# Kernel tuning notes

Measured on AMD Instinct MI355X. Metric: run time of the kernel, lower is better.

The kernel has to match this reference:

```python
import jax, jax.numpy as jnp
import numpy as np

E = 100  # embed_size


def _forward_sentence(noun_emb, subj_cube, obj_cube, words, vs, vo, vt):
    # words: [W] noun ids; vs/vo: [N,2]; vt: [N,3]
    word_sum = noun_emb[words].sum(axis=0)  # [E]
    # gather verb matrices (rows of E*E) in the original cat order
    verb_mats = jnp.concatenate([
        subj_cube[vs[:, 0]],
        obj_cube[vo[:, 0]],
        subj_cube[vt[:, 0]],
        obj_cube[vt[:, 0]],
    ], axis=0).reshape(-1, E, E)  # [4N, E, E]
    arg_vecs = jnp.concatenate([
        noun_emb[vs[:, 1]],
        noun_emb[vo[:, 1]],
        noun_emb[vt[:, 1]],
        noun_emb[vt[:, 2]],
    ], axis=0)  # [4N, E]
    # batched matrix-vector product then reduce over all edges
    verb_arg_sum = jnp.einsum('nij,nj->i', verb_mats, arg_vecs)  # [E]
    return word_sum + verb_arg_sum


def setup_inputs() -> dict:
    key = jax.random.key(0)
    ks = jax.random.split(key, 16)
    n_nouns, n_verbs, hidden = 100000, 5000, 300
    inp = {
        'words1': jax.random.randint(ks[0], (50000,), 0, n_nouns),
        'verb_subj1': jax.random.randint(ks[1], (5000, 2), 0, n_verbs),
        'verb_obj1': jax.random.randint(ks[2], (5000, 2), 0, n_verbs),
        'verb_trans1': jax.random.randint(ks[3], (5000, 3), 0, n_verbs),
        'words2': jax.random.randint(ks[4], (50000,), 0, n_nouns),
        'verb_subj2': jax.random.randint(ks[5], (5000, 2), 0, n_verbs),
        'verb_obj2': jax.random.randint(ks[6], (5000, 2), 0, n_verbs),
        'verb_trans2': jax.random.randint(ks[7], (5000, 3), 0, n_verbs),
        'noun_emb': jax.random.normal(ks[8], (n_nouns, E), jnp.float32) * 0.1,
        'subj_cube': jax.random.normal(ks[9], (n_verbs, E * E), jnp.float32) * 0.02,
        'obj_cube': jax.random.normal(ks[10], (n_verbs, E * E), jnp.float32) * 0.02,
        'W_h': jax.random.normal(ks[11], (hidden, 4 * E), jnp.float32) * 0.05,
        'b_h': jax.random.normal(ks[12], (hidden,), jnp.float32) * 0.05,
        'W_o': jax.random.normal(ks[13], (3, hidden), jnp.float32) * 0.05,
        'b_o': jax.random.normal(ks[14], (3,), jnp.float32) * 0.05,
    }
    return inp


def reference(words1, verb_subj1, verb_obj1, verb_trans1,
              words2, verb_subj2, verb_obj2, verb_trans2,
              noun_emb, subj_cube, obj_cube, W_h, b_h, W_o, b_o):
    emb1 = _forward_sentence(noun_emb, subj_cube, obj_cube, words1, verb_subj1, verb_obj1, verb_trans1)
    emb2 = _forward_sentence(noun_emb, subj_cube, obj_cube, words2, verb_subj2, verb_obj2, verb_trans2)
    mult_dist = emb1 * emb2
    abs_dist = jnp.abs(emb1 - emb2)
    vec_dist = jnp.concatenate([emb1, emb2, mult_dist, abs_dist], axis=0)  # [4E]
    h = jax.nn.sigmoid(vec_dist @ W_h.T + b_h)  # [hidden]
    out = jax.nn.log_softmax(h @ W_o.T + b_o, axis=-1)  # [3]
    return out
```

## Files before the change

### kernel.cpp

```cpp
#include <hip/hip_runtime.h>
#include <math.h>

#define E 100
#define NV 5000
#define NPART 64
#define CAP 16


__global__ void init_kernel(int* __restrict__ count, float* __restrict__ partial) {
    int p = blockIdx.x * blockDim.x + threadIdx.x;
    if (p < 4 * NV) count[p] = 0;
    if (p < NPART * 2 * E) partial[p] = 0.f;
}

__global__ void bucket_build_kernel(const int* __restrict__ vs1, const int* __restrict__ vo1,
                                    const int* __restrict__ vt1,
                                    const int* __restrict__ vs2, const int* __restrict__ vo2,
                                    const int* __restrict__ vt2,
                                    int* __restrict__ count, int* __restrict__ bucket) {
    int p = blockIdx.x * blockDim.x + threadIdx.x;
    if (p >= 40000) return;
    int sent = p / 20000;
    int r = p - sent * 20000;
    int kind = r / 5000;
    int idx = r - kind * 5000;
    const int* vs = sent ? vs2 : vs1;
    const int* vo = sent ? vo2 : vo1;
    const int* vt = sent ? vt2 : vt1;
    int verb, arg, cube;
    if (kind == 0)      { verb = vs[idx * 2]; arg = vs[idx * 2 + 1]; cube = 0; }
    else if (kind == 1) { verb = vo[idx * 2]; arg = vo[idx * 2 + 1]; cube = 1; }
    else if (kind == 2) { verb = vt[idx * 3]; arg = vt[idx * 3 + 1]; cube = 0; }
    else                { verb = vt[idx * 3]; arg = vt[idx * 3 + 2]; cube = 1; }
    int slot = (cube * 2 + sent) * NV + verb;
    int pos = atomicAdd(&count[slot], 1);
    if (pos < CAP) bucket[slot * CAP + pos] = arg;
}

__global__ __launch_bounds__(512) void word_sum_kernel(const int* __restrict__ w1,
                                                       const int* __restrict__ w2,
                                                       const float* __restrict__ noun_emb,
                                                       float* __restrict__ partial) {
    __shared__ int wid[400];
    __shared__ float wred[E];
    int b = blockIdx.x;
    int sent = b / 125;
    int cb = b - sent * 125;
    const int* words = sent ? w2 : w1;
    int t = threadIdx.x;
    if (t < 400) wid[t] = words[cb * 400 + t];
    if (t >= 400 && t < 500) wred[t - 400] = 0.f;
    __syncthreads();
    if (t < 500) {
        int wl = t / 25, k = t - (t / 25) * 25;
        const float4* ne4 = (const float4*)noun_emb;
        float ax = 0.f, ay = 0.f, az = 0.f, aw = 0.f;
        #pragma unroll
        for (int j = 0; j < 20; j++) {
            float4 v = ne4[wid[wl * 20 + j] * 25 + k];
            ax += v.x; ay += v.y; az += v.z; aw += v.w;
        }
        atomicAdd(&wred[k * 4 + 0], ax);
        atomicAdd(&wred[k * 4 + 1], ay);
        atomicAdd(&wred[k * 4 + 2], az);
        atomicAdd(&wred[k * 4 + 3], aw);
    }
    __syncthreads();
    if (t < 100) atomicAdd(&partial[((b & (NPART - 1)) * 2 + sent) * E + t], wred[t]);
}

__global__ __launch_bounds__(512) void cube_pass_kernel(const float* __restrict__ subj,
                                                        const float* __restrict__ obj,
                                                        const float* __restrict__ noun_emb,
                                                        const int* __restrict__ count,
                                                        const int* __restrict__ bucket,
                                                        float* __restrict__ partial) {
    __shared__ float xs[5][2][E];
    __shared__ float yred[2][E];

    int b = blockIdx.x;
    int cube = b / 1000;
    int vbase = (b - cube * 1000) * 5;
    int t = threadIdx.x;

    if (t < 200) yred[t / 100][t % 100] = 0.f;

    if (t < 500) {
        int g = t / 100, i = t - (t / 100) * 100;
        #pragma unroll
        for (int s = 0; s < 2; s++) {
            int slot = (cube * 2 + s) * NV + vbase + g;
            int n = count[slot]; if (n > CAP) n = CAP;
            const int4* b4 = (const int4*)(bucket + slot * CAP);
            int4 q0 = b4[0], q1 = b4[1], q2 = b4[2], q3 = b4[3];
            int ids[16] = {q0.x,q0.y,q0.z,q0.w, q1.x,q1.y,q1.z,q1.w,
                           q2.x,q2.y,q2.z,q2.w, q3.x,q3.y,q3.z,q3.w};
            float acc = 0.f;
            #pragma unroll
            for (int j = 0; j < CAP; j++)
                if (j < n) acc += noun_emb[ids[j] * E + i];
            xs[g][s][i] = acc;
        }
    }
    __syncthreads();

    if (t < 500) {
        int tr = t / 25, c = t - (t / 25) * 25;
        float4 xf1[5], xf2[5];
        #pragma unroll
        for (int v = 0; v < 5; v++) {
            xf1[v] = *(const float4*)&xs[v][0][c * 4];
            xf2[v] = *(const float4*)&xs[v][1][c * 4];
        }
        const float* cb = cube ? obj : subj;
        const float4* base = (const float4*)cb + (size_t)vbase * 2500;
        #pragma unroll
        for (int it = 0; it < 5; it++) {
            float a1 = 0.f, a2 = 0.f;
            #pragma unroll
            for (int v = 0; v < 5; v++) {
                float4 m = base[v * 2500 + it * 500 + t];
                a1 += m.x * xf1[v].x + m.y * xf1[v].y + m.z * xf1[v].z + m.w * xf1[v].w;
                a2 += m.x * xf2[v].x + m.y * xf2[v].y + m.z * xf2[v].z + m.w * xf2[v].w;
            }
            int row = it * 20 + tr;
            atomicAdd(&yred[0][row], a1);
            atomicAdd(&yred[1][row], a2);
        }
    }
    __syncthreads();

    if (t < 200) {
        int s = t / 100, i = t - (t / 100) * 100;
        atomicAdd(&partial[((b & (NPART - 1)) * 2 + s) * E + i], yred[s][i]);
    }
}

__global__ __launch_bounds__(512) void hidden_kernel(const float* __restrict__ partial,
                                                     const float* __restrict__ W_h,
                                                     const float* __restrict__ b_h,
                                                     float* __restrict__ hbuf) {
    __shared__ float vds[4 * E];
    int t = threadIdx.x;
    if (t < 200) {
        int s = t / 100, i = t - (t / 100) * 100;
        float sum = 0.f;
        #pragma unroll 8
        for (int p = 0; p < NPART; p++) sum += partial[(p * 2 + s) * E + i];
        vds[s * E + i] = sum;
    }
    __syncthreads();
    if (t < E) {
        float e1 = vds[t], e2 = vds[E + t];
        vds[2 * E + t] = e1 * e2;
        vds[3 * E + t] = fabsf(e1 - e2);
    }
    __syncthreads();
    int wave = t >> 6, lane = t & 63;
    int h = blockIdx.x * 8 + wave;
    if (h < 300) {
        const float4* w4 = (const float4*)(W_h + (size_t)h * 4 * E);
        const float4* v4 = (const float4*)vds;
        float4 w = w4[lane], v = v4[lane];
        float acc = w.x * v.x + w.y * v.y + w.z * v.z + w.w * v.w;
        if (lane < 36) {
            float4 w2 = w4[lane + 64], v2 = v4[lane + 64];
            acc += w2.x * v2.x + w2.y * v2.y + w2.z * v2.z + w2.w * v2.w;
        }
        #pragma unroll
        for (int off = 32; off > 0; off >>= 1) acc += __shfl_down(acc, off);
        if (lane == 0) hbuf[h] = 1.f / (1.f + expf(-(acc + b_h[h])));
    }
}

__global__ __launch_bounds__(512) void out_kernel(const float* __restrict__ hbuf,
                                                  const float* __restrict__ W_o,
                                                  const float* __restrict__ b_o,
                                                  float* __restrict__ out) {
    __shared__ float hs[300];
    __shared__ float o[3];
    int t = threadIdx.x;
    if (t < 300) hs[t] = hbuf[t];
    __syncthreads();
    int wave = t >> 6, lane = t & 63;
    if (wave < 3) {
        float acc = 0.f;
        #pragma unroll
        for (int j = 0; j < 5; j++) {
            int h = lane + j * 64;
            if (h < 300) acc += W_o[wave * 300 + h] * hs[h];
        }
        #pragma unroll
        for (int off = 32; off > 0; off >>= 1) acc += __shfl_down(acc, off);
        if (lane == 0) o[wave] = acc + b_o[wave];
    }
    __syncthreads();
    if (t == 0) {
        float m = fmaxf(o[0], fmaxf(o[1], o[2]));
        float l = logf(expf(o[0] - m) + expf(o[1] - m) + expf(o[2] - m)) + m;
        out[0] = o[0] - l;
        out[1] = o[1] - l;
        out[2] = o[2] - l;
    }
}

extern "C" void kernel_launch(void* const* d_in, const int* in_sizes, int n_in,
                              void* d_out, int out_size, void* d_ws, size_t ws_size,
                              hipStream_t stream) {
    const int* words1 = (const int*)d_in[0];
    const int* vs1    = (const int*)d_in[1];
    const int* vo1    = (const int*)d_in[2];
    const int* vt1    = (const int*)d_in[3];
    const int* words2 = (const int*)d_in[4];
    const int* vs2    = (const int*)d_in[5];
    const int* vo2    = (const int*)d_in[6];
    const int* vt2    = (const int*)d_in[7];
    const float* noun_emb = (const float*)d_in[8];
    const float* subj     = (const float*)d_in[9];
    const float* obj      = (const float*)d_in[10];
    const float* W_h      = (const float*)d_in[11];
    const float* b_h      = (const float*)d_in[12];
    const float* W_o      = (const float*)d_in[13];
    const float* b_o      = (const float*)d_in[14];
    float* out = (float*)d_out;

    int*   count   = (int*)d_ws;
    int*   bucket  = count + 4 * NV;
    float* partial = (float*)(bucket + 4 * NV * CAP);
    float* hbuf    = partial + NPART * 2 * E;

    init_kernel<<<(4 * NV + 255) / 256, 256, 0, stream>>>(count, partial);
    bucket_build_kernel<<<(40000 + 255) / 256, 256, 0, stream>>>(
        vs1, vo1, vt1, vs2, vo2, vt2, count, bucket);
    word_sum_kernel<<<250, 512, 0, stream>>>(words1, words2, noun_emb, partial);
    cube_pass_kernel<<<2000, 512, 0, stream>>>(subj, obj, noun_emb, count, bucket, partial);
    hidden_kernel<<<38, 512, 0, stream>>>(partial, W_h, b_h, hbuf);
    out_kernel<<<1, 512, 0, stream>>>(hbuf, W_o, b_o, out);
}
```

Before: 469.9 us.

## Precompute argument-sum vectors and stream cube rows one thread per row

Adds a separate kernel that gathers and sums the noun embeddings for each verb slot into a dense buffer A. The fused cube kernel is replaced by a streaming kernel in which each thread computes one 100-wide row dot product against both sentences' A vectors. The goal is to drop the shared-memory staging and block syncs and let more blocks stream the 400 MB of verb cubes. In exchange, each lane reads its own contiguous 400-byte row, so loads within a wavefront are not coalesced across lanes. Every thread also issues its own global atomicAdds into the partial buffer instead of reducing within the block first.

Result: slower. 542.3 us (+15.4%).

```diff
diff --git a/kernel.cpp b/kernel.cpp
--- a/kernel.cpp
+++ b/kernel.cpp
@@ -37,6 +37,27 @@
     if (pos < CAP) bucket[slot * CAP + pos] = arg;
 }
 
+__global__ void build_A_kernel(const int* __restrict__ count, const int* __restrict__ bucket,
+                               const float* __restrict__ noun_emb, float* __restrict__ A) {
+    int p = blockIdx.x * blockDim.x + threadIdx.x;
+    if (p >= 4 * NV * 25) return;
+    int slot = p / 25, c = p - (p / 25) * 25;
+    int n = count[slot]; if (n > CAP) n = CAP;
+    const int4* b4 = (const int4*)(bucket + slot * CAP);
+    int4 q0 = b4[0], q1 = b4[1], q2 = b4[2], q3 = b4[3];
+    int ids[16] = {q0.x,q0.y,q0.z,q0.w, q1.x,q1.y,q1.z,q1.w,
+                   q2.x,q2.y,q2.z,q2.w, q3.x,q3.y,q3.z,q3.w};
+    const float4* ne4 = (const float4*)noun_emb;
+    float ax = 0.f, ay = 0.f, az = 0.f, aw = 0.f;
+    #pragma unroll
+    for (int j = 0; j < CAP; j++)
+        if (j < n) {
+            float4 v = ne4[ids[j] * 25 + c];
+            ax += v.x; ay += v.y; az += v.z; aw += v.w;
+        }
+    ((float4*)A)[p] = make_float4(ax, ay, az, aw);
+}
+
 __global__ __launch_bounds__(512) void word_sum_kernel(const int* __restrict__ w1,
                                                        const int* __restrict__ w2,
                                                        const float* __restrict__ noun_emb,
@@ -69,71 +90,39 @@
     if (t < 100) atomicAdd(&partial[((b & (NPART - 1)) * 2 + sent) * E + t], wred[t]);
 }
 
-__global__ __launch_bounds__(512) void cube_pass_kernel(const float* __restrict__ subj,
-                                                        const float* __restrict__ obj,
-                                                        const float* __restrict__ noun_emb,
-                                                        const int* __restrict__ count,
-                                                        const int* __restrict__ bucket,
-                                                        float* __restrict__ partial) {
-    __shared__ float xs[5][2][E];
-    __shared__ float yred[2][E];
-
-    int b = blockIdx.x;
-    int cube = b / 1000;
-    int vbase = (b - cube * 1000) * 5;
-    int t = threadIdx.x;
-
-    if (t < 200) yred[t / 100][t % 100] = 0.f;
-
-    if (t < 500) {
-        int g = t / 100, i = t - (t / 100) * 100;
-        #pragma unroll
-        for (int s = 0; s < 2; s++) {
-            int slot = (cube * 2 + s) * NV + vbase + g;
-            int n = count[slot]; if (n > CAP) n = CAP;
-            const int4* b4 = (const int4*)(bucket + slot * CAP);
-            int4 q0 = b4[0], q1 = b4[1], q2 = b4[2], q3 = b4[3];
-            int ids[16] = {q0.x,q0.y,q0.z,q0.w, q1.x,q1.y,q1.z,q1.w,
-                           q2.x,q2.y,q2.z,q2.w, q3.x,q3.y,q3.z,q3.w};
-            float acc = 0.f;
-            #pragma unroll
-            for (int j = 0; j < CAP; j++)
-                if (j < n) acc += noun_emb[ids[j] * E + i];
-            xs[g][s][i] = acc;
-        }
-    }
-    __syncthreads();
-
-    if (t < 500) {
-        int tr = t / 25, c = t - (t / 25) * 25;
-        float4 xf1[5], xf2[5];
-        #pragma unroll
-        for (int v = 0; v < 5; v++) {
-            xf1[v] = *(const float4*)&xs[v][0][c * 4];
-            xf2[v] = *(const float4*)&xs[v][1][c * 4];
-        }
-        const float* cb = cube ? obj : subj;
-        const float4* base = (const float4*)cb + (size_t)vbase * 2500;
-        #pragma unroll
-        for (int it = 0; it < 5; it++) {
-            float a1 = 0.f, a2 = 0.f;
-            #pragma unroll
-            for (int v = 0; v < 5; v++) {
-                float4 m = base[v * 2500 + it * 500 + t];
-                a1 += m.x * xf1[v].x + m.y * xf1[v].y + m.z * xf1[v].z + m.w * xf1[v].w;
-                a2 += m.x * xf2[v].x + m.y * xf2[v].y + m.z * xf2[v].z + m.w * xf2[v].w;
-            }
-            int row = it * 20 + tr;
-            atomicAdd(&yred[0][row], a1);
-            atomicAdd(&yred[1][row], a2);
-        }
-    }
-    __syncthreads();
-
-    if (t < 200) {
-        int s = t / 100, i = t - (t / 100) * 100;
-        atomicAdd(&partial[((b & (NPART - 1)) * 2 + s) * E + i], yred[s][i]);
-    }
+__global__ __launch_bounds__(256, 4) void cube_stream_kernel(const float* __restrict__ subj,
+                                                             const float* __restrict__ obj,
+                                                             const float* __restrict__ A,
+                                                             float* __restrict__ partial) {
+    int r = blockIdx.x * 256 + threadIdx.x;
+    if (r >= 2 * NV * E) return;
+    int cube = r / (NV * E);
+    int rem = r - cube * (NV * E);
+    int v = rem / E, i = rem - v * E;
+    const float4* row = (const float4*)(cube ? obj : subj) + (size_t)rem * 25;
+    const float4* x1  = (const float4*)A + ((size_t)(cube * 2 + 0) * NV + v) * 25;
+    const float4* x2  = (const float4*)A + ((size_t)(cube * 2 + 1) * NV + v) * 25;
+
+    float a1e = 0.f, a1o = 0.f, a2e = 0.f, a2o = 0.f;
+    #pragma unroll
+    for (int k = 0; k < 24; k += 2) {
+        float4 m0 = row[k],   m1 = row[k + 1];
+        float4 p0 = x1[k],    p1 = x1[k + 1];
+        float4 q0 = x2[k],    q1 = x2[k + 1];
+        a1e += m0.x * p0.x + m0.y * p0.y + m0.z * p0.z + m0.w * p0.w;
+        a1o += m1.x * p1.x + m1.y * p1.y + m1.z * p1.z + m1.w * p1.w;
+        a2e += m0.x * q0.x + m0.y * q0.y + m0.z * q0.z + m0.w * q0.w;
+        a2o += m1.x * q1.x + m1.y * q1.y + m1.z * q1.z + m1.w * q1.w;
+    }
+    {
+        float4 m0 = row[24];
+        float4 p0 = x1[24], q0 = x2[24];
+        a1e += m0.x * p0.x + m0.y * p0.y + m0.z * p0.z + m0.w * p0.w;
+        a2e += m0.x * q0.x + m0.y * q0.y + m0.z * q0.z + m0.w * q0.w;
+    }
+    int sl = (blockIdx.x & (NPART - 1)) * 2;
+    atomicAdd(&partial[(sl + 0) * E + i], a1e + a1o);
+    atomicAdd(&partial[(sl + 1) * E + i], a2e + a2o);
 }
 
 __global__ __launch_bounds__(512) void hidden_kernel(const float* __restrict__ partial,
@@ -226,14 +215,16 @@
 
     int*   count   = (int*)d_ws;
     int*   bucket  = count + 4 * NV;
-    float* partial = (float*)(bucket + 4 * NV * CAP);
+    float* A       = (float*)(bucket + 4 * NV * CAP);
+    float* partial = A + 4 * NV * E;
     float* hbuf    = partial + NPART * 2 * E;
 
     init_kernel<<<(4 * NV + 255) / 256, 256, 0, stream>>>(count, partial);
     bucket_build_kernel<<<(40000 + 255) / 256, 256, 0, stream>>>(
         vs1, vo1, vt1, vs2, vo2, vt2, count, bucket);
+    build_A_kernel<<<(4 * NV * 25 + 255) / 256, 256, 0, stream>>>(count, bucket, noun_emb, A);
     word_sum_kernel<<<250, 512, 0, stream>>>(words1, words2, noun_emb, partial);
-    cube_pass_kernel<<<2000, 512, 0, stream>>>(subj, obj, noun_emb, count, bucket, partial);
+    cube_stream_kernel<<<(2 * NV * E + 255) / 256, 256, 0, stream>>>(subj, obj, A, partial);
     hidden_kernel<<<38, 512, 0, stream>>>(partial, W_h, b_h, hbuf);
     out_kernel<<<1, 512, 0, stream>>>(hbuf, W_o, b_o, out);
 }
```
